# Kernel optimization log

Hardware: AMD Instinct MI355X
Metric: run time of the kernel (lower is better)

Reference implementation:

```python
import math
import jax, jax.numpy as jnp
import numpy as np

B, S, DM, H = 4, 1024, 1024, 16
D = DM // H


def setup_inputs() -> dict:
    key = jax.random.key(0)
    ks = jax.random.split(key, 8)
    q = jax.random.normal(ks[0], (B, S, DM), dtype=jnp.float32)
    k = jax.random.normal(ks[1], (B, S, DM), dtype=jnp.float32)
    v = jax.random.normal(ks[2], (B, S, DM), dtype=jnp.float32)
    w_scale = 0.02
    Wq = jax.random.normal(ks[3], (DM, DM), dtype=jnp.float32) * w_scale
    Wk = jax.random.normal(ks[4], (DM, DM), dtype=jnp.float32) * w_scale
    Wv = jax.random.normal(ks[5], (DM, DM), dtype=jnp.float32) * w_scale
    Wo = jax.random.normal(ks[6], (DM, DM), dtype=jnp.float32) * w_scale
    bq = jnp.zeros((DM,), jnp.float32)
    bk = jnp.zeros((DM,), jnp.float32)
    bv = jnp.zeros((DM,), jnp.float32)
    bo = jnp.zeros((DM,), jnp.float32)
    # mask==1 means masked (upper triangle above the diagonal)
    causal_mask = jnp.triu(jnp.ones((S, S), jnp.int32), k=1)
    return {"q": q, "k": k, "v": v, "Wq": Wq, "bq": bq, "Wk": Wk, "bk": bk,
            "Wv": Wv, "bv": bv, "Wo": Wo, "bo": bo, "causal_mask": causal_mask}


def reference(q, k, v, Wq, bq, Wk, bk, Wv, bv, Wo, bo, causal_mask):
    Bn, Sq, Dm = q.shape
    # projections (torch Linear: x @ W.T + b)
    qh = (q @ Wq.T + bq).reshape(Bn, Sq, H, D).transpose(0, 2, 1, 3)  # [B,H,S,D]
    kh = (k @ Wk.T + bk).reshape(Bn, -1, H, D).transpose(0, 2, 1, 3)
    vh = (v @ Wv.T + bv).reshape(Bn, -1, H, D).transpose(0, 2, 1, 3)
    # NOTE: module divides by sqrt(d_model), not sqrt(d_head)
    score = jnp.einsum('bhqd,bhkd->bhqk', qh, kh) / math.sqrt(Dm)
    score = jnp.where(causal_mask == 1, jnp.float32(-1e9), score)
    attn_weights = jax.nn.softmax(score, axis=-1)  # dropout is identity in eval
    x = jnp.einsum('bhqk,bhkd->bhqd', attn_weights, vh)
    x = x.transpose(0, 2, 1, 3).reshape(Bn, Sq, Dm)
    x = x @ Wo.T + bo
    present = jnp.stack([kh, vh])  # [2,B,H,S,D]
    return (x, present, attn_weights)
```

## Files before the change

kernel.cpp:

```cpp
#include <hip/hip_runtime.h>


typedef __bf16 bf16x8 __attribute__((ext_vector_type(8)));
typedef float f32x4 __attribute__((ext_vector_type(4)));
typedef unsigned short u16;
typedef unsigned int u32;

#define B_ 4
#define S_ 1024
#define DM_ 1024
#define H_ 16
#define D_ 64

static constexpr size_t N_QKV = (size_t)B_ * S_ * DM_;
static constexpr size_t N_W   = (size_t)DM_ * DM_;

static constexpr size_t QB_OFF = 0;
static constexpr size_t KB_OFF = QB_OFF + N_QKV;
static constexpr size_t VB_OFF = KB_OFF + N_QKV;
static constexpr size_t WQ_OFF = VB_OFF + N_QKV;
static constexpr size_t WK_OFF = WQ_OFF + N_W;
static constexpr size_t WV_OFF = WK_OFF + N_W;
static constexpr size_t WO_OFF = WV_OFF + N_W;
static constexpr size_t QH_OFF = WO_OFF + N_W;
static constexpr size_t KH_OFF = QH_OFF + N_QKV;
static constexpr size_t VT_OFF = KH_OFF + N_QKV;
static constexpr size_t XH_OFF = VT_OFF + N_QKV;

static constexpr size_t P0_OFF = N_QKV;
static constexpr size_t P1_OFF = 2 * N_QKV;
static constexpr size_t AW_OFF = 3 * N_QKV;

__device__ __forceinline__ u16 f2bf(float f) {
    u32 u = __float_as_uint(f);
    u += 0x7FFFu + ((u >> 16) & 1u);
    return (u16)(u >> 16);
}

__device__ __forceinline__ f32x4 zero4() {
    f32x4 z = {0.f, 0.f, 0.f, 0.f};
    return z;
}

__device__ __forceinline__ void async16(const void* g, void* lds) {
    __builtin_amdgcn_global_load_lds(
        (__attribute__((address_space(1))) u32*)g,
        (__attribute__((address_space(3))) u32*)lds,
        16, 0, 0);
}

__device__ __forceinline__ int swzf(int f) {
    return f ^ (((f >> 7) & 7) << 4);
}
__device__ __forceinline__ int swz16(int row, int elem) {
    return row * 64 + (elem ^ ((row & 7) << 3));
}

__global__ __launch_bounds__(256) void cvt_kernel(
    const float* __restrict__ q, const float* __restrict__ k, const float* __restrict__ v,
    const float* __restrict__ wq, const float* __restrict__ wk, const float* __restrict__ wv,
    const float* __restrict__ wo, u16* __restrict__ ws)
{
    const int seg = blockIdx.y;
    const float* src; u16* dst; size_t n;
    switch (seg) {
        case 0: src = q;  dst = ws + QB_OFF; n = N_QKV; break;
        case 1: src = k;  dst = ws + KB_OFF; n = N_QKV; break;
        case 2: src = v;  dst = ws + VB_OFF; n = N_QKV; break;
        case 3: src = wq; dst = ws + WQ_OFF; n = N_W;   break;
        case 4: src = wk; dst = ws + WK_OFF; n = N_W;   break;
        case 5: src = wv; dst = ws + WV_OFF; n = N_W;   break;
        default: src = wo; dst = ws + WO_OFF; n = N_W;  break;
    }
    const size_t idx = ((size_t)blockIdx.x * 256 + threadIdx.x) * 4;
    if (idx >= n) return;
    float4 f = *(const float4*)(src + idx);
    u32 p0 = (u32)f2bf(f.x) | ((u32)f2bf(f.y) << 16);
    u32 p1 = (u32)f2bf(f.z) | ((u32)f2bf(f.w) << 16);
    *(uint2*)(dst + idx) = make_uint2(p0, p1);
}

__device__ __forceinline__ void gemm_mainloop(
    const u16* __restrict__ A, const u16* __restrict__ W, int K,
    int row0, int col0, u16* As, u16* Bs, f32x4 (&acc)[4][4])
{
    const int tid = threadIdx.x;
    const int lane = tid & 63;
    const int w = tid >> 6;
    const int wm = w & 1, wn = w >> 1;
    const int l15 = lane & 15;
    const int acol = (lane >> 4) * 8;

    for (int k0 = 0; k0 < K; k0 += 32) {
#pragma unroll
        for (int j = 0; j < 2; ++j) {
            const int f = (j * 256 + tid) * 16;
            const int r = f >> 6, cb = f & 63;
            async16((const char*)A + ((size_t)(row0 + r) * K + k0) * 2 + cb,
                    (char*)As + j * 4096 + w * 1024);
            async16((const char*)W + ((size_t)(col0 + r) * K + k0) * 2 + cb,
                    (char*)Bs + j * 4096 + w * 1024);
        }
        __syncthreads();
        bf16x8 af[4], bfr[4];
#pragma unroll
        for (int t = 0; t < 4; ++t) {
            af[t]  = *(const bf16x8*)(As + (wm * 64 + t * 16 + l15) * 32 + acol);
            bfr[t] = *(const bf16x8*)(Bs + (wn * 64 + t * 16 + l15) * 32 + acol);
        }
#pragma unroll
        for (int tm = 0; tm < 4; ++tm)
#pragma unroll
            for (int tn = 0; tn < 4; ++tn)
                acc[tm][tn] = __builtin_amdgcn_mfma_f32_16x16x32_bf16(
                    af[tm], bfr[tn], acc[tm][tn], 0, 0, 0);
        __syncthreads();
    }
}

__global__ __launch_bounds__(256) void proj_kernel(
    u16* __restrict__ ws, const float* __restrict__ bq, const float* __restrict__ bk,
    const float* __restrict__ bv, float* __restrict__ out)
{
    const int mode = blockIdx.z;
    const u16* A = ws + QB_OFF + (size_t)mode * N_QKV;
    const u16* W = ws + WQ_OFF + (size_t)mode * N_W;
    const float* bias = (mode == 0) ? bq : (mode == 1 ? bk : bv);
    __shared__ __align__(16) u16 smem[128 * 128];
    u16* As = smem;
    u16* Bs = smem + 128 * 32;
    u16* T  = smem;
    f32x4 acc[4][4];
#pragma unroll
    for (int i = 0; i < 4; ++i)
#pragma unroll
        for (int j = 0; j < 4; ++j) acc[i][j] = zero4();

    const int row0 = blockIdx.x * 128, col0 = blockIdx.y * 128;
    gemm_mainloop(A, W, DM_, row0, col0, As, Bs, acc);

    const int tid = threadIdx.x;
    const int lane = tid & 63, w = tid >> 6;
    const int wm = w & 1, wn = w >> 1;
    const int quad = lane >> 4, l15 = lane & 15;
#pragma unroll
    for (int tm = 0; tm < 4; ++tm)
#pragma unroll
        for (int tn = 0; tn < 4; ++tn)
#pragma unroll
            for (int i = 0; i < 4; ++i) {
                const int m = row0 + wm * 64 + tm * 16 + quad * 4 + i;
                const int n = col0 + wn * 64 + tn * 16 + l15;
                const float val = acc[tm][tn][i] + bias[n];
                const int b = m >> 10, s = m & (S_ - 1);
                const int h = n >> 6, d = n & 63;
                const size_t hidx = (((size_t)b * H_ + h) * S_ + s) * D_ + d;
                if (mode == 0) {
                    ws[QH_OFF + hidx] = f2bf(val);
                } else if (mode == 1) {
                    out[P0_OFF + hidx] = val;
                    ws[KH_OFF + hidx] = f2bf(val);
                } else {
                    out[P1_OFF + hidx] = val;
                    const int r = wn * 64 + tn * 16 + l15;
                    const int c = wm * 64 + tm * 16 + quad * 4 + i;
                    T[r * 128 + (c ^ ((r & 15) << 3))] = f2bf(val);
                }
            }

    if (mode == 2) {
        __syncthreads();
        const int b = row0 >> 10;
        const int s0 = row0 & (S_ - 1);
#pragma unroll
        for (int p = 0; p < 8; ++p) {
            const int r = p * 16 + (tid >> 4);
            const int c0 = (tid & 15) * 8;
            const int n = col0 + r;
            const int h = n >> 6, d = n & 63;
            bf16x8 vv = *(const bf16x8*)(T + r * 128 + (c0 ^ ((r & 15) << 3)));
            *(bf16x8*)(ws + VT_OFF + (((size_t)b * H_ + h) * D_ + d) * S_ + s0 + c0) = vv;
        }
    }
}

__global__ __launch_bounds__(256) void attn_kernel(u16* __restrict__ ws, float* __restrict__ out)
{
    const int qt = (S_ / 64 - 1) - blockIdx.x;
    const int h  = blockIdx.y;
    const int b  = blockIdx.z;
    const int bh = b * H_ + h;
    const int q0 = qt * 64;

    const u16* Qg  = ws + QH_OFF + ((size_t)bh * S_ + q0) * D_;
    const u16* Kg  = ws + KH_OFF + (size_t)bh * S_ * D_;
    const u16* Vtg = ws + VT_OFF + (size_t)bh * D_ * S_;
    float* AW = out + AW_OFF + ((size_t)bh * S_ + q0) * S_;
    u16* XH = ws + XH_OFF;

    __shared__ __align__(16) u16 Qs[64 * 64];
    __shared__ __align__(16) u16 Ks[64 * 64];
    __shared__ __align__(16) u16 Vs[64 * 64];
    __shared__ __align__(16) u16 Ps[4][16 * 64];

    const int tid = threadIdx.x;
    const int lane = tid & 63;
    const int w = tid >> 6;
    const int quad = lane >> 4, l15 = lane & 15;

#pragma unroll
    for (int j = 0; j < 2; ++j) {
        const int f = (j * 256 + tid) * 16;
        async16((const char*)Qg + swzf(f), (char*)Qs + j * 4096 + w * 1024);
    }
    __syncthreads();

    bf16x8 aq[2];
#pragma unroll
    for (int kk = 0; kk < 2; ++kk)
        aq[kk] = *(const bf16x8*)(Qs + swz16(w * 16 + l15, kk * 32 + quad * 8));

    const int ntiles = qt + 1;
    const float scale = 0.03125f;
    const int qrow = q0 + w * 16 + quad * 4;

    float ps[4] = {0.f, 0.f, 0.f, 0.f};
    for (int t = 0; t < ntiles; ++t) {
        __syncthreads();
#pragma unroll
        for (int j = 0; j < 2; ++j) {
            const int f = (j * 256 + tid) * 16;
            async16((const char*)Kg + (size_t)t * 8192 + swzf(f),
                    (char*)Ks + j * 4096 + w * 1024);
        }
        __syncthreads();
        f32x4 sa[4];
        sa[0] = sa[1] = sa[2] = sa[3] = zero4();
        __builtin_amdgcn_s_setprio(1);
#pragma unroll
        for (int kk = 0; kk < 2; ++kk) {
#pragma unroll
            for (int n = 0; n < 4; ++n) {
                bf16x8 bk = *(const bf16x8*)(Ks + swz16(n * 16 + l15, kk * 32 + quad * 8));
                sa[n] = __builtin_amdgcn_mfma_f32_16x16x32_bf16(aq[kk], bk, sa[n], 0, 0, 0);
            }
        }
        __builtin_amdgcn_s_setprio(0);
#pragma unroll
        for (int n = 0; n < 4; ++n) {
            const int kcol = t * 64 + n * 16 + l15;
#pragma unroll
            for (int i = 0; i < 4; ++i) {
                float e = (kcol <= qrow + i) ? __expf(sa[n][i] * scale) : 0.f;
                ps[i] += e;
            }
        }
    }

    float rinv[4];
#pragma unroll
    for (int i = 0; i < 4; ++i) {
        float s = ps[i];
        s += __shfl_xor(s, 1);
        s += __shfl_xor(s, 2);
        s += __shfl_xor(s, 4);
        s += __shfl_xor(s, 8);
        rinv[i] = 1.f / s;
    }

    f32x4 oacc[4];
    oacc[0] = oacc[1] = oacc[2] = oacc[3] = zero4();

    for (int t = 0; t < ntiles; ++t) {
        __syncthreads();
#pragma unroll
        for (int j = 0; j < 2; ++j) {
            const int f = (j * 256 + tid) * 16;
            async16((const char*)Kg + (size_t)t * 8192 + swzf(f),
                    (char*)Ks + j * 4096 + w * 1024);
            const int d = f >> 7;
            const int cb = (f & 127) ^ ((d & 7) << 4);
            async16((const char*)Vtg + (size_t)d * (S_ * 2) + (size_t)t * 128 + cb,
                    (char*)Vs + j * 4096 + w * 1024);
        }
        __syncthreads();
        f32x4 sa[4];
        sa[0] = sa[1] = sa[2] = sa[3] = zero4();
        __builtin_amdgcn_s_setprio(1);
#pragma unroll
        for (int kk = 0; kk < 2; ++kk) {
#pragma unroll
            for (int n = 0; n < 4; ++n) {
                bf16x8 bk = *(const bf16x8*)(Ks + swz16(n * 16 + l15, kk * 32 + quad * 8));
                sa[n] = __builtin_amdgcn_mfma_f32_16x16x32_bf16(aq[kk], bk, sa[n], 0, 0, 0);
            }
        }
        __builtin_amdgcn_s_setprio(0);
#pragma unroll
        for (int n = 0; n < 4; ++n) {
            const int kcol = t * 64 + n * 16 + l15;
#pragma unroll
            for (int i = 0; i < 4; ++i) {
                float e = (kcol <= qrow + i) ? __expf(sa[n][i] * scale) : 0.f;
                float wgt = e * rinv[i];
                AW[(size_t)(w * 16 + quad * 4 + i) * S_ + kcol] = wgt;
                Ps[w][swz16(quad * 4 + i, n * 16 + l15)] = f2bf(wgt);
            }
        }
        __builtin_amdgcn_s_setprio(1);
#pragma unroll
        for (int kk = 0; kk < 2; ++kk) {
            bf16x8 ap = *(const bf16x8*)(&Ps[w][swz16(l15, kk * 32 + quad * 8)]);
#pragma unroll
            for (int n = 0; n < 4; ++n) {
                bf16x8 bv = *(const bf16x8*)(Vs + swz16(n * 16 + l15, kk * 32 + quad * 8));
                oacc[n] = __builtin_amdgcn_mfma_f32_16x16x32_bf16(ap, bv, oacc[n], 0, 0, 0);
            }
        }
        __builtin_amdgcn_s_setprio(0);
    }

#pragma unroll
    for (int n = 0; n < 4; ++n)
#pragma unroll
        for (int i = 0; i < 4; ++i) {
            const int qq = q0 + w * 16 + quad * 4 + i;
            const int dc = h * 64 + n * 16 + l15;
            XH[((size_t)b * S_ + qq) * DM_ + dc] = f2bf(oacc[n][i]);
        }

    const int zc0 = ntiles * 64;
    const int Z = S_ - zc0;
    if (Z > 0) {
        const int total = 64 * Z;
        for (int idx = tid * 4; idx < total; idx += 1024) {
            const int r = idx / Z, c = idx - r * Z;
            *(float4*)(&AW[(size_t)r * S_ + zc0 + c]) = make_float4(0.f, 0.f, 0.f, 0.f);
        }
    }
}

__global__ __launch_bounds__(256) void outproj_kernel(
    u16* __restrict__ ws, const float* __restrict__ bo, float* __restrict__ out)
{
    const u16* A = ws + XH_OFF;
    const u16* W = ws + WO_OFF;
    __shared__ __align__(16) u16 As[128 * 32];
    __shared__ __align__(16) u16 Bs[128 * 32];
    f32x4 acc[4][4];
#pragma unroll
    for (int i = 0; i < 4; ++i)
#pragma unroll
        for (int j = 0; j < 4; ++j) acc[i][j] = zero4();

    const int row0 = blockIdx.x * 128, col0 = blockIdx.y * 128;
    gemm_mainloop(A, W, DM_, row0, col0, As, Bs, acc);

    const int lane = threadIdx.x & 63, w = threadIdx.x >> 6;
    const int wm = w & 1, wn = w >> 1;
    const int quad = lane >> 4, l15 = lane & 15;
#pragma unroll
    for (int tm = 0; tm < 4; ++tm)
#pragma unroll
        for (int tn = 0; tn < 4; ++tn)
#pragma unroll
            for (int i = 0; i < 4; ++i) {
                const int m = row0 + wm * 64 + tm * 16 + quad * 4 + i;
                const int n = col0 + wn * 64 + tn * 16 + l15;
                out[(size_t)m * DM_ + n] = acc[tm][tn][i] + bo[n];
            }
}

extern "C" void kernel_launch(void* const* d_in, const int* in_sizes, int n_in,
                              void* d_out, int out_size, void* d_ws, size_t ws_size,
                              hipStream_t stream) {
    const float* q  = (const float*)d_in[0];
    const float* k  = (const float*)d_in[1];
    const float* v  = (const float*)d_in[2];
    const float* Wq = (const float*)d_in[3];
    const float* bq = (const float*)d_in[4];
    const float* Wk = (const float*)d_in[5];
    const float* bk = (const float*)d_in[6];
    const float* Wv = (const float*)d_in[7];
    const float* bv = (const float*)d_in[8];
    const float* Wo = (const float*)d_in[9];
    const float* bo = (const float*)d_in[10];

    u16* ws = (u16*)d_ws;
    float* out = (float*)d_out;
    dim3 blk(256);

    cvt_kernel<<<dim3(4096, 7, 1), blk, 0, stream>>>(q, k, v, Wq, Wk, Wv, Wo, ws);
    proj_kernel<<<dim3(32, 8, 3), blk, 0, stream>>>(ws, bq, bk, bv, out);
    attn_kernel<<<dim3(S_ / 64, H_, B_), blk, 0, stream>>>(ws, out);
    outproj_kernel<<<dim3(32, 8, 1), blk, 0, stream>>>(ws, bo, out);
}
```

Before: 492.3 us.

## Move causal-zero fill of attention weights to separate kernel and remap attention grid across XCDs

```diff
diff --git a/kernel.cpp b/kernel.cpp
--- a/kernel.cpp
+++ b/kernel.cpp
@@ -78,6 +78,30 @@
     u32 p0 = (u32)f2bf(f.x) | ((u32)f2bf(f.y) << 16);
     u32 p1 = (u32)f2bf(f.z) | ((u32)f2bf(f.w) << 16);
     *(uint2*)(dst + idx) = make_uint2(p0, p1);
+}
+
+__global__ __launch_bounds__(256) void awzero_kernel(float* __restrict__ out)
+{
+    const int tid = threadIdx.x;
+#pragma unroll
+    for (int u = 0; u < 2; ++u) {
+        const int st = blockIdx.x * 2 + u;
+        const int bh = st / 120;
+        int rem = st - bh * 120;
+        int qt = 0;
+        while (rem >= 15 - qt) { rem -= 15 - qt; ++qt; }
+        const int q0 = qt * 64;
+        const int col0 = (qt + 1 + rem) * 64;
+        float* base = out + AW_OFF + ((size_t)bh * S_ + q0) * S_;
+        const int row = tid >> 2;
+        const int cg = (tid & 3) * 16;
+        float4 z = make_float4(0.f, 0.f, 0.f, 0.f);
+        float* p = base + (size_t)row * S_ + col0 + cg;
+        *(float4*)(p)      = z;
+        *(float4*)(p + 4)  = z;
+        *(float4*)(p + 8)  = z;
+        *(float4*)(p + 12) = z;
+    }
 }
 
 __device__ __forceinline__ void gemm_mainloop(
@@ -186,10 +210,13 @@
 
 __global__ __launch_bounds__(256) void attn_kernel(u16* __restrict__ ws, float* __restrict__ out)
 {
-    const int qt = (S_ / 64 - 1) - blockIdx.x;
-    const int h  = blockIdx.y;
-    const int b  = blockIdx.z;
-    const int bh = b * H_ + h;
+    const int flat = blockIdx.x;
+    const int xcd = flat & 7;
+    const int pos = flat >> 3;
+    const int gp  = xcd * 128 + pos;
+    const int bh  = gp >> 4;
+    const int qt  = 15 - (gp & 15);
+    const int b = bh >> 4, h = bh & 15;
     const int q0 = qt * 64;
 
     const u16* Qg  = ws + QH_OFF + ((size_t)bh * S_ + q0) * D_;
@@ -328,16 +355,6 @@
             const int dc = h * 64 + n * 16 + l15;
             XH[((size_t)b * S_ + qq) * DM_ + dc] = f2bf(oacc[n][i]);
         }
-
-    const int zc0 = ntiles * 64;
-    const int Z = S_ - zc0;
-    if (Z > 0) {
-        const int total = 64 * Z;
-        for (int idx = tid * 4; idx < total; idx += 1024) {
-            const int r = idx / Z, c = idx - r * Z;
-            *(float4*)(&AW[(size_t)r * S_ + zc0 + c]) = make_float4(0.f, 0.f, 0.f, 0.f);
-        }
-    }
 }
 
 __global__ __launch_bounds__(256) void outproj_kernel(
@@ -391,7 +408,8 @@
     dim3 blk(256);
 
     cvt_kernel<<<dim3(4096, 7, 1), blk, 0, stream>>>(q, k, v, Wq, Wk, Wv, Wo, ws);
+    awzero_kernel<<<dim3(3840, 1, 1), blk, 0, stream>>>(out);
     proj_kernel<<<dim3(32, 8, 3), blk, 0, stream>>>(ws, bq, bk, bv, out);
-    attn_kernel<<<dim3(S_ / 64, H_, B_), blk, 0, stream>>>(ws, out);
+    attn_kernel<<<dim3(1024, 1, 1), blk, 0, stream>>>(ws, out);
     outproj_kernel<<<dim3(32, 8, 1), blk, 0, stream>>>(ws, bo, out);
 }
```

After: 493.8 us. About the same (+0.3%).
